# Performance work log

Measured on AMD Instinct MI355X. Metric: run time of the kernel, lower is better.

Reference implementation:

```python
import jax, jax.numpy as jnp
import numpy as np

GROUP_SIZE = 256
QMAX = 7.0   # int4 symmetric: clamp to [-8, 7], scale from max_abs/7
QMIN = -8.0
EPS = 1e-9


def _dequantized_weight(weight):
    """Symmetric int4 group quantization (group_size=256 along input dim),
    then dequantize. Matches group_quantize_tensor_symmetric + qc4w matmul math.
    weight: [out, in] float32."""
    O, I = weight.shape
    wg = weight.reshape(O, I // GROUP_SIZE, GROUP_SIZE)
    scale = jnp.maximum(jnp.max(jnp.abs(wg), axis=-1, keepdims=True) / QMAX, EPS)
    w_int = jnp.clip(jnp.round(wg / scale), QMIN, QMAX)
    return (w_int * scale).reshape(O, I)


def setup_inputs() -> dict:
    key = jax.random.key(0)
    k1, k2 = jax.random.split(key)
    x = jax.random.normal(k1, (1, 16, 4096), dtype=jnp.float32)
    weight = jax.random.normal(k2, (14336, 4096), dtype=jnp.float32) * 0.02
    return {"x": x, "weight": weight}


def reference(x, weight):
    # x: [1, S, I]; weight: [O, I]
    w_dq = _dequantized_weight(weight)           # [O, I]
    xs = x[0]                                    # squeeze batch (asserted == 1)
    out = jnp.einsum('si,oi->so', xs, w_dq)     # [S, O]
    return out[None, ...]                        # [1, S, O]
```

## Files before the change

kernel.cpp:

```cpp
#include <hip/hip_runtime.h>


constexpr int O_DIM = 14336;
constexpr int I_DIM = 4096;
constexpr int S_DIM = 16;
constexpr int GS    = 256;
constexpr int NSPL  = 2;
constexpr int GPS   = (I_DIM / GS) / NSPL;
constexpr int RPW   = 4;
constexpr int RPB   = 8;

__global__ __launch_bounds__(256, 4)
void qlin_kernel(const float* __restrict__ x,
                 const float* __restrict__ w,
                 float* __restrict__ out)
{
    __shared__ float part[NSPL - 1][2][64];

    const int tid  = threadIdx.x;
    const int lane = tid & 63;
    const int wv   = tid >> 6;
    const int rw   = wv & 1;
    const int sp   = wv >> 1;
    const int row0 = blockIdx.x * RPB + rw * RPW;
    const size_t ibase = (size_t)sp * (I_DIM / NSPL);

    const float* wp = w + (size_t)row0 * I_DIM + ibase + lane * 4;
    const float* xp = x + ibase + lane * 4;

    float acc[RPW][S_DIM];
#pragma unroll
    for (int r = 0; r < RPW; ++r)
#pragma unroll
        for (int s = 0; s < S_DIM; ++s) acc[r][s] = 0.0f;

    float4 wcur[RPW], wnext[RPW];
#pragma unroll
    for (int r = 0; r < RPW; ++r)
        wcur[r] = *reinterpret_cast<const float4*>(wp + (size_t)r * I_DIM);

    for (int g = 0; g < GPS; ++g) {
        const int base = g * GS;

        if (g + 1 < GPS) {
#pragma unroll
            for (int r = 0; r < RPW; ++r)
                wnext[r] = *reinterpret_cast<const float4*>(
                    wp + (size_t)r * I_DIM + base + GS);
        }

        float4 xv[4], xn[4];
#pragma unroll
        for (int k = 0; k < 4; ++k)
            xv[k] = *reinterpret_cast<const float4*>(xp + (size_t)k * I_DIM + base);

        float4 dq[RPW];
#pragma unroll
        for (int r = 0; r < RPW; ++r) {
            float4 v = wcur[r];
            float m = fmaxf(fmaxf(fabsf(v.x), fabsf(v.y)),
                            fmaxf(fabsf(v.z), fabsf(v.w)));
#pragma unroll
            for (int off = 1; off < 64; off <<= 1)
                m = fmaxf(m, __shfl_xor(m, off, 64));
            float scale = fmaxf(m * (1.0f / 7.0f), 1e-9f);
            float invs  = __builtin_amdgcn_rcpf(scale);
            dq[r].x = rintf(v.x * invs) * scale;
            dq[r].y = rintf(v.y * invs) * scale;
            dq[r].z = rintf(v.z * invs) * scale;
            dq[r].w = rintf(v.w * invs) * scale;
        }

#pragma unroll
        for (int sb = 0; sb < S_DIM; sb += 4) {
            if (sb + 4 < S_DIM) {
#pragma unroll
                for (int k = 0; k < 4; ++k)
                    xn[k] = *reinterpret_cast<const float4*>(
                        xp + (size_t)(sb + 4 + k) * I_DIM + base);
            }
#pragma unroll
            for (int k = 0; k < 4; ++k) {
                const int s = sb + k;
#pragma unroll
                for (int r = 0; r < RPW; ++r) {
                    acc[r][s] = fmaf(dq[r].x, xv[k].x, acc[r][s]);
                    acc[r][s] = fmaf(dq[r].y, xv[k].y, acc[r][s]);
                    acc[r][s] = fmaf(dq[r].z, xv[k].z, acc[r][s]);
                    acc[r][s] = fmaf(dq[r].w, xv[k].w, acc[r][s]);
                }
            }
#pragma unroll
            for (int k = 0; k < 4; ++k) xv[k] = xn[k];
        }

#pragma unroll
        for (int r = 0; r < RPW; ++r) wcur[r] = wnext[r];
    }

    float a[64];
#pragma unroll
    for (int r = 0; r < RPW; ++r)
#pragma unroll
        for (int s = 0; s < S_DIM; ++s) a[(r << 4) | s] = acc[r][s];

#pragma unroll
    for (int m = 32; m >= 1; m >>= 1) {
        const bool hi = (lane & m) != 0;
#pragma unroll
        for (int j = 0; j < m; ++j) {
            float snd  = hi ? a[j] : a[j + m];
            float rcv  = __shfl_xor(snd, m, 64);
            float kept = hi ? a[j + m] : a[j];
            a[j] = kept + rcv;
        }
    }
    float v = a[0];

    if (sp == 1) part[0][rw][lane] = v;
    __syncthreads();
    if (sp == 0) {
        v += part[0][rw][lane];
        const int r = lane >> 4, s = lane & 15;
        out[s * O_DIM + (row0 + r)] = v;
    }
}

extern "C" void kernel_launch(void* const* d_in, const int* in_sizes, int n_in,
                              void* d_out, int out_size, void* d_ws, size_t ws_size,
                              hipStream_t stream) {
    const float* x = (const float*)d_in[0];
    const float* w = (const float*)d_in[1];
    float* out = (float*)d_out;
    dim3 grid(O_DIM / RPB);
    dim3 block(256);
    qlin_kernel<<<grid, block, 0, stream>>>(x, w, out);
}
```

Baseline: 384.9 us.

## Stage activations in shared memory and use 14-wave blocks without input split

Replaces the 2-way input-dimension split and per-thread global loads of x with large 896-thread blocks that cooperatively stage 1024-wide x phases into LDS and read them from there. Each wave now covers the full input dimension for its 4 rows, which removes the cross-wave partial-sum combine. The aim is to cut redundant global and L2 traffic for x and raise data reuse. In exchange, the grid shrinks to 256 blocks of 14 waves, roughly one block per CU, with barriers per phase and 64KB of LDS, so occupancy and latency hiding for the weight stream may suffer.

```diff
diff --git a/kernel.cpp b/kernel.cpp
--- a/kernel.cpp
+++ b/kernel.cpp
@@ -1,32 +1,31 @@
 #include <hip/hip_runtime.h>
 
 
-constexpr int O_DIM = 14336;
-constexpr int I_DIM = 4096;
-constexpr int S_DIM = 16;
-constexpr int GS    = 256;
-constexpr int NSPL  = 2;
-constexpr int GPS   = (I_DIM / GS) / NSPL;
-constexpr int RPW   = 4;
-constexpr int RPB   = 8;
+constexpr int O_DIM  = 14336;
+constexpr int I_DIM  = 4096;
+constexpr int S_DIM  = 16;
+constexpr int GS     = 256;
+constexpr int NG     = I_DIM / GS;
+constexpr int RPW    = 4;
+constexpr int NWAVE  = 14;
+constexpr int RPB    = RPW * NWAVE;
+constexpr int PH_I   = 1024;
+constexpr int NPH    = I_DIM / PH_I;
+constexpr int GPP    = PH_I / GS;
 
-__global__ __launch_bounds__(256, 4)
+__global__ __launch_bounds__(896)
 void qlin_kernel(const float* __restrict__ x,
                  const float* __restrict__ w,
                  float* __restrict__ out)
 {
-    __shared__ float part[NSPL - 1][2][64];
+    __shared__ float xs[S_DIM][PH_I];
 
     const int tid  = threadIdx.x;
     const int lane = tid & 63;
     const int wv   = tid >> 6;
-    const int rw   = wv & 1;
-    const int sp   = wv >> 1;
-    const int row0 = blockIdx.x * RPB + rw * RPW;
-    const size_t ibase = (size_t)sp * (I_DIM / NSPL);
+    const int row0 = blockIdx.x * RPB + wv * RPW;
 
-    const float* wp = w + (size_t)row0 * I_DIM + ibase + lane * 4;
-    const float* xp = x + ibase + lane * 4;
+    const float* wp = w + (size_t)row0 * I_DIM + lane * 4;
 
     float acc[RPW][S_DIM];
 #pragma unroll
@@ -39,63 +38,59 @@
     for (int r = 0; r < RPW; ++r)
         wcur[r] = *reinterpret_cast<const float4*>(wp + (size_t)r * I_DIM);
 
-    for (int g = 0; g < GPS; ++g) {
-        const int base = g * GS;
+    for (int p = 0; p < NPH; ++p) {
+        for (int j = tid; j < S_DIM * (PH_I / 4); j += 896) {
+            const int s  = j >> 8;
+            const int i4 = (j & 255) * 4;
+            float4 v = *reinterpret_cast<const float4*>(
+                &x[(size_t)s * I_DIM + p * PH_I + i4]);
+            *reinterpret_cast<float4*>(&xs[s][i4]) = v;
+        }
+        __syncthreads();
 
-        if (g + 1 < GPS) {
+        for (int g = 0; g < GPP; ++g) {
+            const int G = p * GPP + g;
+
+            if (G + 1 < NG) {
 #pragma unroll
-            for (int r = 0; r < RPW; ++r)
-                wnext[r] = *reinterpret_cast<const float4*>(
-                    wp + (size_t)r * I_DIM + base + GS);
-        }
-
-        float4 xv[4], xn[4];
-#pragma unroll
-        for (int k = 0; k < 4; ++k)
-            xv[k] = *reinterpret_cast<const float4*>(xp + (size_t)k * I_DIM + base);
-
-        float4 dq[RPW];
-#pragma unroll
-        for (int r = 0; r < RPW; ++r) {
-            float4 v = wcur[r];
-            float m = fmaxf(fmaxf(fabsf(v.x), fabsf(v.y)),
-                            fmaxf(fabsf(v.z), fabsf(v.w)));
-#pragma unroll
-            for (int off = 1; off < 64; off <<= 1)
-                m = fmaxf(m, __shfl_xor(m, off, 64));
-            float scale = fmaxf(m * (1.0f / 7.0f), 1e-9f);
-            float invs  = __builtin_amdgcn_rcpf(scale);
-            dq[r].x = rintf(v.x * invs) * scale;
-            dq[r].y = rintf(v.y * invs) * scale;
-            dq[r].z = rintf(v.z * invs) * scale;
-            dq[r].w = rintf(v.w * invs) * scale;
-        }
+                for (int r = 0; r < RPW; ++r)
+                    wnext[r] = *reinterpret_cast<const float4*>(
+                        wp + (size_t)r * I_DIM + (G + 1) * GS);
+            }
 
 #pragma unroll
-        for (int sb = 0; sb < S_DIM; sb += 4) {
-            if (sb + 4 < S_DIM) {
+            for (int r = 0; r < RPW; ++r) {
+                float4 v = wcur[r];
+                float m = fmaxf(fmaxf(fabsf(v.x), fabsf(v.y)),
+                                fmaxf(fabsf(v.z), fabsf(v.w)));
 #pragma unroll
-                for (int k = 0; k < 4; ++k)
-                    xn[k] = *reinterpret_cast<const float4*>(
-                        xp + (size_t)(sb + 4 + k) * I_DIM + base);
+                for (int off = 1; off < 64; off <<= 1)
+                    m = fmaxf(m, __shfl_xor(m, off, 64));
+                float scale = fmaxf(m * (1.0f / 7.0f), 1e-9f);
+                float invs  = 1.0f / scale;
+                wcur[r].x = rintf(v.x * invs) * scale;
+                wcur[r].y = rintf(v.y * invs) * scale;
+                wcur[r].z = rintf(v.z * invs) * scale;
+                wcur[r].w = rintf(v.w * invs) * scale;
             }
+
+            const int xb = g * GS + lane * 4;
 #pragma unroll
-            for (int k = 0; k < 4; ++k) {
-                const int s = sb + k;
+            for (int s = 0; s < S_DIM; ++s) {
+                float4 xv = *reinterpret_cast<const float4*>(&xs[s][xb]);
 #pragma unroll
                 for (int r = 0; r < RPW; ++r) {
-                    acc[r][s] = fmaf(dq[r].x, xv[k].x, acc[r][s]);
-                    acc[r][s] = fmaf(dq[r].y, xv[k].y, acc[r][s]);
-                    acc[r][s] = fmaf(dq[r].z, xv[k].z, acc[r][s]);
-                    acc[r][s] = fmaf(dq[r].w, xv[k].w, acc[r][s]);
+                    acc[r][s] = fmaf(wcur[r].x, xv.x, acc[r][s]);
+                    acc[r][s] = fmaf(wcur[r].y, xv.y, acc[r][s]);
+                    acc[r][s] = fmaf(wcur[r].z, xv.z, acc[r][s]);
+                    acc[r][s] = fmaf(wcur[r].w, xv.w, acc[r][s]);
                 }
             }
-#pragma unroll
-            for (int k = 0; k < 4; ++k) xv[k] = xn[k];
-        }
 
 #pragma unroll
-        for (int r = 0; r < RPW; ++r) wcur[r] = wnext[r];
+            for (int r = 0; r < RPW; ++r) wcur[r] = wnext[r];
+        }
+        __syncthreads();
     }
 
     float a[64];
@@ -115,14 +110,9 @@
             a[j] = kept + rcv;
         }
     }
-    float v = a[0];
-
-    if (sp == 1) part[0][rw][lane] = v;
-    __syncthreads();
-    if (sp == 0) {
-        v += part[0][rw][lane];
+    {
         const int r = lane >> 4, s = lane & 15;
-        out[s * O_DIM + (row0 + r)] = v;
+        out[s * O_DIM + (row0 + r)] = a[0];
     }
 }
 
@@ -133,6 +123,6 @@
     const float* w = (const float*)d_in[1];
     float* out = (float*)d_out;
     dim3 grid(O_DIM / RPB);
-    dim3 block(256);
+    dim3 block(896);
     qlin_kernel<<<grid, block, 0, stream>>>(x, w, out);
 }
```

After: 339.9 us. 11.7% less time.
